# Kernel tuning notes

Hardware: AMD Instinct MI355X
Metric: run time of the kernel (lower is better)

The kernel has to match this reference:

```python
import jax, jax.numpy as jnp
import numpy as np

B, K, D, S, E = 256, 512, 64, 100000, 20000  # batch, knowledge_n, low_dim, student_n, exer_n


def setup_inputs() -> dict:
    key = jax.random.key(0)
    ks = jax.random.split(key, 10)
    stu_id = jax.random.randint(ks[0], (B,), 0, S)
    exer_id = jax.random.randint(ks[1], (B,), 0, E)
    kn_emb = jax.random.uniform(ks[2], (B, K), dtype=jnp.float32)
    # learned parameters (xavier-ish scale)
    stu_table = jax.random.normal(ks[3], (S, D), dtype=jnp.float32) * 0.05
    exer_table = jax.random.normal(ks[4], (E, D), dtype=jnp.float32) * 0.05
    kn_table = jax.random.normal(ks[5], (K, D), dtype=jnp.float32) * 0.05
    W1 = jax.random.normal(ks[6], (K, K + D), dtype=jnp.float32) * (2.0 / (2 * K + D)) ** 0.5
    W2 = jax.random.normal(ks[7], (K, K + D), dtype=jnp.float32) * (2.0 / (2 * K + D)) ** 0.5
    W3 = jax.random.normal(ks[8], (1, K), dtype=jnp.float32) * (2.0 / (K + 1)) ** 0.5
    b3 = jnp.zeros((1,), dtype=jnp.float32)
    return {"stu_id": stu_id, "exer_id": exer_id, "kn_emb": kn_emb,
            "stu_table": stu_table, "exer_table": exer_table, "kn_table": kn_table,
            "W1": W1, "W2": W2, "W3": W3, "b3": b3}


def reference(stu_id, exer_id, kn_emb, stu_table, exer_table, kn_table, W1, W2, W3, b3):
    k = kn_table.shape[0]  # knowledge_n
    # sigmoid(stu_emb @ kn_table.T): (B, K) per-concept proficiency / difficulty
    stu = jax.nn.sigmoid(stu_table[stu_id] @ kn_table.T)
    exer = jax.nn.sigmoid(exer_table[exer_id] @ kn_table.T)
    # Linear on cat([repeated stu/exer vec, kn_vector]) decomposes: split W into
    # the first K columns (acting on the batch vector, constant over the K axis)
    # and the last D columns (acting on kn_table, constant over batch).
    pref = jax.nn.sigmoid((stu @ W1[:, :k].T)[:, None, :] + (kn_table @ W1[:, k:].T)[None, :, :])  # (B,K,K)
    diff = jax.nn.sigmoid((exer @ W2[:, :k].T)[:, None, :] + (kn_table @ W2[:, k:].T)[None, :, :])  # (B,K,K)
    o = jax.nn.sigmoid(jnp.einsum('bkn,n->bk', pref - diff, W3[0]) + b3)  # (B,K)
    sum_out = jnp.sum(o * kn_emb, axis=1, keepdims=True)  # (B,1)
    count = jnp.sum(kn_emb, axis=1, keepdims=True)
    return sum_out / count
```

## Files before the change

kernel.cpp:

```cpp
#include <hip/hip_runtime.h>

#define B_ 256
#define K_ 512
#define D_ 64
#define KD_ 576
#define LOG2E 1.44269504088896340736f

typedef float v4f __attribute__((ext_vector_type(4)));
typedef short bf16x8 __attribute__((ext_vector_type(8)));
typedef float f32x16 __attribute__((ext_vector_type(16)));

#define ZERO16 {0.f,0.f,0.f,0.f,0.f,0.f,0.f,0.f,0.f,0.f,0.f,0.f,0.f,0.f,0.f,0.f}

__device__ __forceinline__ float fexp2(float x) {
#if __has_builtin(__builtin_amdgcn_exp2f)
    return __builtin_amdgcn_exp2f(x);
#else
    float r; asm("v_exp_f32 %0, %1" : "=v"(r) : "v"(x)); return r;
#endif
}
__device__ __forceinline__ float frcp(float x) {
#if __has_builtin(__builtin_amdgcn_rcpf)
    return __builtin_amdgcn_rcpf(x);
#else
    float r; asm("v_rcp_f32 %0, %1" : "=v"(r) : "v"(x)); return r;
#endif
}
__device__ __forceinline__ float fsig(float x) {
    return frcp(1.0f + fexp2(-LOG2E * x));
}
__device__ __forceinline__ ushort f2bf(float f) {
    union { float f; unsigned u; } v; v.f = f;
    return (ushort)((v.u + 0x7FFFu + ((v.u >> 16) & 1u)) >> 16);
}
__device__ __forceinline__ bf16x8 ldcvt8(const float* p) {
    float4 a = *(const float4*)p;
    float4 b = *(const float4*)(p + 4);
    bf16x8 r;
    r[0] = (short)f2bf(a.x); r[1] = (short)f2bf(a.y);
    r[2] = (short)f2bf(a.z); r[3] = (short)f2bf(a.w);
    r[4] = (short)f2bf(b.x); r[5] = (short)f2bf(b.y);
    r[6] = (short)f2bf(b.z); r[7] = (short)f2bf(b.w);
    return r;
}

__global__ void __launch_bounds__(256) kS(const int* __restrict__ sid,
                                          const int* __restrict__ eid,
                                          const float* __restrict__ stu_t,
                                          const float* __restrict__ exer_t,
                                          const float* __restrict__ kn_t,
                                          ushort* __restrict__ Sbu) {
    const int bid = blockIdx.x, t = threadIdx.x;
    const int l = t & 63, w = t >> 6;
    const int dk = (l >> 5) * 8;
    const int tab = bid >> 5, bt = (bid >> 3) & 3, nt = bid & 7;
    const int b0 = bt * 64, n0 = nt * 64;
    const int brow = b0 + (w & 1) * 32 + (l & 31);
    const int ncol = n0 + (w >> 1) * 32 + (l & 31);
    const int id = (tab ? eid : sid)[brow];
    const float* ar = (tab ? exer_t : stu_t) + (size_t)id * D_;
    const float* br = kn_t + (size_t)ncol * D_;
    f32x16 acc = ZERO16;
#pragma unroll
    for (int kk = 0; kk < 4; kk++) {
        bf16x8 a = ldcvt8(ar + kk * 16 + dk);
        bf16x8 b = ldcvt8(br + kk * 16 + dk);
        acc = __builtin_amdgcn_mfma_f32_32x32x16_bf16(a, b, acc, 0, 0, 0);
    }
    ushort* So = Sbu + (size_t)tab * B_ * K_;
#pragma unroll
    for (int r = 0; r < 16; r++) {
        const int row = (r & 3) + 8 * (r >> 2) + 4 * (l >> 5);
        So[(size_t)(b0 + (w & 1) * 32 + row) * K_ + ncol] = f2bf(fsig(acc[r]));
    }
}

__global__ void __launch_bounds__(256) kEF(const ushort* __restrict__ Sbu,
                                           const float* __restrict__ W1,
                                           const float* __restrict__ W2,
                                           const float* __restrict__ kn_t,
                                           float* __restrict__ E,
                                           float* __restrict__ FT1,
                                           float* __restrict__ FT2) {
    __shared__ float shm[4224];
    const int bid = blockIdx.x, t = threadIdx.x;
    const int l = t & 63, w = t >> 6;
    if (bid < 256) {
        const int mat = bid >> 7, bt = (bid >> 4) & 7, nt = bid & 15;
        const int b0 = bt * 32, n0 = nt * 32;
        const int arow = b0 + (l & 31);
        const int nrow = n0 + (l & 31);
        const int koff = w * 128 + (l >> 5) * 8;
        const short* Sp = (const short*)Sbu + (size_t)(mat * B_ + arow) * K_ + koff;
        const float* Wp = (mat ? W2 : W1) + (size_t)nrow * KD_ + koff;
        f32x16 acc = ZERO16;
#pragma unroll
        for (int kk = 0; kk < 8; kk++) {
            bf16x8 a = *(const bf16x8*)(Sp + kk * 16);
            bf16x8 b = ldcvt8(Wp + kk * 16);
            acc = __builtin_amdgcn_mfma_f32_32x32x16_bf16(a, b, acc, 0, 0, 0);
        }
#pragma unroll
        for (int r = 0; r < 16; r++) {
            const int row = (r & 3) + 8 * (r >> 2) + 4 * (l >> 5);
            shm[w * 1056 + row * 33 + (l & 31)] = acc[r];
        }
        __syncthreads();
#pragma unroll
        for (int i = 0; i < 4; i++) {
            const int o = i * 256 + t;
            const int row = (o >> 5) & 31, col = o & 31;
            const float v = shm[row * 33 + col] + shm[1056 + row * 33 + col]
                          + shm[2112 + row * 33 + col] + shm[3168 + row * 33 + col];
            E[(size_t)mat * B_ * K_ + (size_t)(b0 + row) * K_ + n0 + col]
                = fexp2(-LOG2E * v);
        }
    } else {
        const int fid = bid - 256;
        const int mat = fid >> 6, kt = (fid >> 3) & 7, nt = fid & 7;
        const int k0 = kt * 64, n0 = nt * 64;
        const int krow = k0 + (w & 1) * 32 + (l & 31);
        const int ncol = n0 + (w >> 1) * 32 + (l & 31);
        const int dk = (l >> 5) * 8;
        const float* Wm = mat ? W2 : W1;
        const float* ar = kn_t + (size_t)krow * D_;
        const float* br = Wm + (size_t)ncol * KD_ + K_;
        f32x16 acc = ZERO16;
#pragma unroll
        for (int kk = 0; kk < 4; kk++) {
            bf16x8 a = ldcvt8(ar + kk * 16 + dk);
            bf16x8 b = ldcvt8(br + kk * 16 + dk);
            acc = __builtin_amdgcn_mfma_f32_32x32x16_bf16(a, b, acc, 0, 0, 0);
        }
        const int nl_ = (w >> 1) * 32 + (l & 31);
#pragma unroll
        for (int r = 0; r < 16; r++) {
            const int row = (r & 3) + 8 * (r >> 2) + 4 * (l >> 5);
            shm[nl_ * 65 + (w & 1) * 32 + row] = fexp2(-LOG2E * acc[r]);
        }
        __syncthreads();
        float* Fo = mat ? FT2 : FT1;
#pragma unroll
        for (int i = 0; i < 16; i++) {
            const int q = i * 256 + t;
            const int r_ = q >> 6, c_ = q & 63;
            Fo[(size_t)(n0 + r_) * K_ + k0 + c_] = shm[r_ * 65 + c_];
        }
    }
}

__global__ void __launch_bounds__(512) kMain(const float* __restrict__ FT1,
                                             const float* __restrict__ FT2,
                                             const float* __restrict__ Ebase,
                                             const float* __restrict__ W3,
                                             float* __restrict__ pPart) {
    __shared__ float es[2][64][8];
    __shared__ float sacc[3][2][16][64];
    const int t = threadIdx.x, l = t & 63, w = t >> 6;
    const int kg = blockIdx.x, bG = blockIdx.y, ns = blockIdx.z;
    const int b0 = bG * 8, n0 = ns * 64;
    const int k = kg * 256 + l * 4;
    const int bh = w & 1, nq = w >> 1;

#pragma unroll
    for (int it = 0; it < 2; it++) {
        const int i = it * 512 + t;
        const int n = i & 63, b = (i >> 6) & 7, mat = i >> 9;
        es[mat][n][b] = Ebase[(size_t)mat * B_ * K_ + (size_t)(b0 + b) * K_ + n0 + n];
    }
    __syncthreads();

    const float* f1p = FT1 + (size_t)(n0 + nq * 16) * K_ + k;
    const float* f2p = FT2 + (size_t)(n0 + nq * 16) * K_ + k;
    const float* w3p = W3 + n0 + nq * 16;

    v4f acc[4];
#pragma unroll
    for (int b = 0; b < 4; b++) acc[b] = (v4f){0.f, 0.f, 0.f, 0.f};

#pragma unroll 4
    for (int nl = 0; nl < 16; nl++) {
        const v4f f1 = *(const v4f*)(f1p + (size_t)nl * K_);
        const v4f f2 = *(const v4f*)(f2p + (size_t)nl * K_);
        const float w3n = w3p[nl];
        const v4f e1 = *(const v4f*)&es[0][nq * 16 + nl][bh * 4];
        const v4f e2 = *(const v4f*)&es[1][nq * 16 + nl][bh * 4];
#pragma unroll
        for (int b = 0; b < 4; b++) {
            const v4f pd = e1[b] * f1 + 1.0f;
            const v4f qd = e2[b] * f2 + 1.0f;
            const v4f den = pd * qd;
            const v4f num = (qd - pd) * w3n;
            const float dxy = den.x * den.y, dzw = den.z * den.w;
            const float rxy = frcp(dxy), rzw = frcp(dzw);
            v4f rc;
            rc.x = rxy * den.y; rc.y = rxy * den.x;
            rc.z = rzw * den.w; rc.w = rzw * den.z;
            acc[b] += num * rc;
        }
    }

    if (nq != 0) {
#pragma unroll
        for (int b = 0; b < 4; b++)
#pragma unroll
            for (int c = 0; c < 4; c++)
                sacc[nq - 1][bh][b * 4 + c][l] = acc[b][c];
    }
    __syncthreads();
    if (nq == 0) {
#pragma unroll
        for (int b = 0; b < 4; b++) {
            v4f s = acc[b];
#pragma unroll
            for (int q = 0; q < 3; q++) {
                s.x += sacc[q][bh][b * 4 + 0][l];
                s.y += sacc[q][bh][b * 4 + 1][l];
                s.z += sacc[q][bh][b * 4 + 2][l];
                s.w += sacc[q][bh][b * 4 + 3][l];
            }
            *(v4f*)(pPart + ((size_t)ns * B_ + b0 + bh * 4 + b) * K_ + k) = s;
        }
    }
}

__global__ void __launch_bounds__(256) kFin(const float* __restrict__ pPart,
                                            const float* __restrict__ kn_emb,
                                            const float* __restrict__ b3,
                                            float* __restrict__ out) {
    const int t = threadIdx.x, l = t & 63, w = t >> 6;
    const int b = blockIdx.x * 4 + w;
    const float b3v = b3[0];
    const float* ke = kn_emb + (size_t)b * K_;
    float num = 0.f, den = 0.f;
#pragma unroll
    for (int c = 0; c < 8; c++) {
        const int kk = c * 64 + l;
        float sv = 0.f;
#pragma unroll
        for (int s = 0; s < 8; s++)
            sv += pPart[((size_t)s * B_ + b) * K_ + kk];
        const float kv = ke[kk];
        num = fmaf(fsig(sv + b3v), kv, num);
        den += kv;
    }
#pragma unroll
    for (int off = 32; off; off >>= 1) {
        num += __shfl_xor(num, off, 64);
        den += __shfl_xor(den, off, 64);
    }
    if (l == 0) out[b] = num / den;
}

extern "C" void kernel_launch(void* const* d_in, const int* in_sizes, int n_in,
                              void* d_out, int out_size, void* d_ws, size_t ws_size,
                              hipStream_t stream) {
    const int*   stu_id     = (const int*)d_in[0];
    const int*   exer_id    = (const int*)d_in[1];
    const float* kn_emb     = (const float*)d_in[2];
    const float* stu_table  = (const float*)d_in[3];
    const float* exer_table = (const float*)d_in[4];
    const float* kn_table   = (const float*)d_in[5];
    const float* W1         = (const float*)d_in[6];
    const float* W2         = (const float*)d_in[7];
    const float* W3         = (const float*)d_in[8];
    const float* b3         = (const float*)d_in[9];
    float* out = (float*)d_out;

    float* ws = (float*)d_ws;
    float* FT1   = ws;
    float* FT2   = FT1 + (size_t)K_ * K_;
    float* E     = FT2 + (size_t)K_ * K_;
    ushort* Sbu  = (ushort*)(E + 2 * (size_t)B_ * K_);
    float* pPart = (float*)(Sbu + 2 * (size_t)B_ * K_);

    kS<<<64, 256, 0, stream>>>(stu_id, exer_id, stu_table, exer_table,
                               kn_table, Sbu);
    kEF<<<384, 256, 0, stream>>>(Sbu, W1, W2, kn_table, E, FT1, FT2);
    kMain<<<dim3(2, 32, 8), 512, 0, stream>>>(FT1, FT2, E, W3, pPart);
    kFin<<<64, 256, 0, stream>>>(pPart, kn_emb, b3, out);
}
```

Baseline: 37.19 us.

## Run main pairwise sigmoid-difference loop in packed fp16 with fp16 F tables

Stores the exp-factor tables FT1/FT2 as packed fp16 and rewrites the main kernel to compute pd/qd/den/numerator and reciprocals with packed half2 arithmetic and v_rcp_f16. The work split also changes: each block now covers 4 batch rows, with waves partitioned over n, and partials are reduced through shared memory. The final kernel uses one block per batch row. The aim is to halve table bandwidth and double ALU throughput in the dominant loop, at the cost of fp16 accumulation error and possible overflow or precision loss in the products.

```diff
diff --git a/kernel.cpp b/kernel.cpp
--- a/kernel.cpp
+++ b/kernel.cpp
@@ -9,6 +9,7 @@
 typedef float v4f __attribute__((ext_vector_type(4)));
 typedef short bf16x8 __attribute__((ext_vector_type(8)));
 typedef float f32x16 __attribute__((ext_vector_type(16)));
+typedef _Float16 h2 __attribute__((ext_vector_type(2)));
 
 #define ZERO16 {0.f,0.f,0.f,0.f,0.f,0.f,0.f,0.f,0.f,0.f,0.f,0.f,0.f,0.f,0.f,0.f}
 
@@ -29,9 +30,21 @@
 __device__ __forceinline__ float fsig(float x) {
     return frcp(1.0f + fexp2(-LOG2E * x));
 }
+__device__ __forceinline__ _Float16 hrcp(_Float16 x) {
+    _Float16 r; asm("v_rcp_f16 %0, %1" : "=v"(r) : "v"(x)); return r;
+}
 __device__ __forceinline__ ushort f2bf(float f) {
     union { float f; unsigned u; } v; v.f = f;
     return (ushort)((v.u + 0x7FFFu + ((v.u >> 16) & 1u)) >> 16);
+}
+__device__ __forceinline__ unsigned f2h_dup(float x) {
+    const _Float16 h = (_Float16)x;
+    const h2 p = {h, h};
+    return __builtin_bit_cast(unsigned, p);
+}
+__device__ __forceinline__ unsigned f2h_pair(float a, float b) {
+    const h2 p = {(_Float16)a, (_Float16)b};
+    return __builtin_bit_cast(unsigned, p);
 }
 __device__ __forceinline__ bf16x8 ldcvt8(const float* p) {
     float4 a = *(const float4*)p;
@@ -80,8 +93,8 @@
                                            const float* __restrict__ W2,
                                            const float* __restrict__ kn_t,
                                            float* __restrict__ E,
-                                           float* __restrict__ FT1,
-                                           float* __restrict__ FT2) {
+                                           unsigned* __restrict__ FT1h,
+                                           unsigned* __restrict__ FT2h) {
     __shared__ float shm[4224];
     const int bid = blockIdx.x, t = threadIdx.x;
     const int l = t & 63, w = t >> 6;
@@ -139,88 +152,105 @@
             shm[nl_ * 65 + (w & 1) * 32 + row] = fexp2(-LOG2E * acc[r]);
         }
         __syncthreads();
-        float* Fo = mat ? FT2 : FT1;
-#pragma unroll
-        for (int i = 0; i < 16; i++) {
+        unsigned* Fo = mat ? FT2h : FT1h;
+#pragma unroll
+        for (int i = 0; i < 8; i++) {
             const int q = i * 256 + t;
-            const int r_ = q >> 6, c_ = q & 63;
-            Fo[(size_t)(n0 + r_) * K_ + k0 + c_] = shm[r_ * 65 + c_];
-        }
-    }
-}
-
-__global__ void __launch_bounds__(512) kMain(const float* __restrict__ FT1,
-                                             const float* __restrict__ FT2,
+            const int r_ = q >> 5, c_ = q & 31;
+            Fo[(size_t)(n0 + r_) * (K_ / 2) + (k0 >> 1) + c_] =
+                f2h_pair(shm[r_ * 65 + 2 * c_], shm[r_ * 65 + 2 * c_ + 1]);
+        }
+    }
+}
+
+__global__ void __launch_bounds__(512) kMain(const unsigned* __restrict__ FT1h,
+                                             const unsigned* __restrict__ FT2h,
                                              const float* __restrict__ Ebase,
                                              const float* __restrict__ W3,
                                              float* __restrict__ pPart) {
-    __shared__ float es[2][64][8];
-    __shared__ float sacc[3][2][16][64];
+    __shared__ unsigned es[2][64][4];
+    __shared__ unsigned w3s[64];
+    __shared__ float sacc[4][4][64][8];
     const int t = threadIdx.x, l = t & 63, w = t >> 6;
     const int kg = blockIdx.x, bG = blockIdx.y, ns = blockIdx.z;
-    const int b0 = bG * 8, n0 = ns * 64;
-    const int k = kg * 256 + l * 4;
-    const int bh = w & 1, nq = w >> 1;
-
-#pragma unroll
-    for (int it = 0; it < 2; it++) {
-        const int i = it * 512 + t;
-        const int n = i & 63, b = (i >> 6) & 7, mat = i >> 9;
-        es[mat][n][b] = Ebase[(size_t)mat * B_ * K_ + (size_t)(b0 + b) * K_ + n0 + n];
-    }
+    const int b0 = bG * 4, n0 = ns * 64;
+
+    {
+        const int n = t & 63, b = (t >> 6) & 3, mat = t >> 8;
+        const float ev = Ebase[(size_t)mat * B_ * K_ + (size_t)(b0 + b) * K_ + n0 + n];
+        es[mat][n][b] = f2h_dup(ev);
+    }
+    if (t < 64) w3s[t] = f2h_dup(W3[n0 + t]);
     __syncthreads();
 
-    const float* f1p = FT1 + (size_t)(n0 + nq * 16) * K_ + k;
-    const float* f2p = FT2 + (size_t)(n0 + nq * 16) * K_ + k;
-    const float* w3p = W3 + n0 + nq * 16;
-
-    v4f acc[4];
-#pragma unroll
-    for (int b = 0; b < 4; b++) acc[b] = (v4f){0.f, 0.f, 0.f, 0.f};
-
-#pragma unroll 4
-    for (int nl = 0; nl < 16; nl++) {
-        const v4f f1 = *(const v4f*)(f1p + (size_t)nl * K_);
-        const v4f f2 = *(const v4f*)(f2p + (size_t)nl * K_);
-        const float w3n = w3p[nl];
-        const v4f e1 = *(const v4f*)&es[0][nq * 16 + nl][bh * 4];
-        const v4f e2 = *(const v4f*)&es[1][nq * 16 + nl][bh * 4];
+    const int kq = kg * 128 + l * 2;
+    const unsigned* f1p = FT1h + (size_t)n0 * (K_ / 2) + kq;
+    const unsigned* f2p = FT2h + (size_t)n0 * (K_ / 2) + kq;
+
+    const h2 one2 = {(_Float16)1.0f, (_Float16)1.0f};
+    h2 acc[4][2];
+#pragma unroll
+    for (int b = 0; b < 4; b++) {
+        acc[b][0] = (h2){(_Float16)0.0f, (_Float16)0.0f};
+        acc[b][1] = (h2){(_Float16)0.0f, (_Float16)0.0f};
+    }
+
+    const int nbase = w * 8;
+#pragma unroll
+    for (int nl = 0; nl < 8; nl++) {
+        const int n = nbase + nl;
+        const uint2 f1r = *(const uint2*)(f1p + (size_t)n * (K_ / 2));
+        const uint2 f2r = *(const uint2*)(f2p + (size_t)n * (K_ / 2));
+        const h2 f1a = __builtin_bit_cast(h2, f1r.x);
+        const h2 f1b = __builtin_bit_cast(h2, f1r.y);
+        const h2 f2a = __builtin_bit_cast(h2, f2r.x);
+        const h2 f2b = __builtin_bit_cast(h2, f2r.y);
+        const h2 w3h = __builtin_bit_cast(h2, w3s[n]);
+        const uint4 e1r = *(const uint4*)&es[0][n][0];
+        const uint4 e2r = *(const uint4*)&es[1][n][0];
+        const unsigned e1u[4] = {e1r.x, e1r.y, e1r.z, e1r.w};
+        const unsigned e2u[4] = {e2r.x, e2r.y, e2r.z, e2r.w};
 #pragma unroll
         for (int b = 0; b < 4; b++) {
-            const v4f pd = e1[b] * f1 + 1.0f;
-            const v4f qd = e2[b] * f2 + 1.0f;
-            const v4f den = pd * qd;
-            const v4f num = (qd - pd) * w3n;
-            const float dxy = den.x * den.y, dzw = den.z * den.w;
-            const float rxy = frcp(dxy), rzw = frcp(dzw);
-            v4f rc;
-            rc.x = rxy * den.y; rc.y = rxy * den.x;
-            rc.z = rzw * den.w; rc.w = rzw * den.z;
-            acc[b] += num * rc;
-        }
-    }
-
-    if (nq != 0) {
-#pragma unroll
-        for (int b = 0; b < 4; b++)
-#pragma unroll
-            for (int c = 0; c < 4; c++)
-                sacc[nq - 1][bh][b * 4 + c][l] = acc[b][c];
+            const h2 e1 = __builtin_bit_cast(h2, e1u[b]);
+            const h2 e2 = __builtin_bit_cast(h2, e2u[b]);
+            {
+                const h2 pd = e1 * f1a + one2;
+                const h2 qd = e2 * f2a + one2;
+                const h2 den = pd * qd;
+                const h2 nw = (qd - pd) * w3h;
+                const h2 rc = {hrcp(den.x), hrcp(den.y)};
+                acc[b][0] += nw * rc;
+            }
+            {
+                const h2 pd = e1 * f1b + one2;
+                const h2 qd = e2 * f2b + one2;
+                const h2 den = pd * qd;
+                const h2 nw = (qd - pd) * w3h;
+                const h2 rc = {hrcp(den.x), hrcp(den.y)};
+                acc[b][1] += nw * rc;
+            }
+        }
+    }
+
+#pragma unroll
+    for (int b = 0; b < 4; b++) {
+        sacc[b][0][l][w] = (float)acc[b][0].x;
+        sacc[b][1][l][w] = (float)acc[b][0].y;
+        sacc[b][2][l][w] = (float)acc[b][1].x;
+        sacc[b][3][l][w] = (float)acc[b][1].y;
     }
     __syncthreads();
-    if (nq == 0) {
-#pragma unroll
-        for (int b = 0; b < 4; b++) {
-            v4f s = acc[b];
-#pragma unroll
-            for (int q = 0; q < 3; q++) {
-                s.x += sacc[q][bh][b * 4 + 0][l];
-                s.y += sacc[q][bh][b * 4 + 1][l];
-                s.z += sacc[q][bh][b * 4 + 2][l];
-                s.w += sacc[q][bh][b * 4 + 3][l];
-            }
-            *(v4f*)(pPart + ((size_t)ns * B_ + b0 + bh * 4 + b) * K_ + k) = s;
-        }
+#pragma unroll
+    for (int o = 0; o < 2; o++) {
+        const int flat = o * 512 + t;
+        const int b = flat >> 8, rem = flat & 255, l2 = rem >> 2, c = rem & 3;
+        const v4f lo = *(const v4f*)&sacc[b][c][l2][0];
+        const v4f hi = *(const v4f*)&sacc[b][c][l2][4];
+        const float s = ((lo.x + lo.y) + (lo.z + lo.w))
+                      + ((hi.x + hi.y) + (hi.z + hi.w));
+        const int k = kg * 256 + l2 * 4 + c;
+        pPart[((size_t)ns * B_ + b0 + b) * K_ + k] = s;
     }
 }
 
@@ -228,19 +258,19 @@
                                             const float* __restrict__ kn_emb,
                                             const float* __restrict__ b3,
                                             float* __restrict__ out) {
+    __shared__ float rn[4], rd[4];
     const int t = threadIdx.x, l = t & 63, w = t >> 6;
-    const int b = blockIdx.x * 4 + w;
+    const int b = blockIdx.x;
     const float b3v = b3[0];
-    const float* ke = kn_emb + (size_t)b * K_;
     float num = 0.f, den = 0.f;
 #pragma unroll
-    for (int c = 0; c < 8; c++) {
-        const int kk = c * 64 + l;
+    for (int c = 0; c < 2; c++) {
+        const int kk = c * 256 + t;
         float sv = 0.f;
 #pragma unroll
         for (int s = 0; s < 8; s++)
             sv += pPart[((size_t)s * B_ + b) * K_ + kk];
-        const float kv = ke[kk];
+        const float kv = kn_emb[(size_t)b * K_ + kk];
         num = fmaf(fsig(sv + b3v), kv, num);
         den += kv;
     }
@@ -249,7 +279,10 @@
         num += __shfl_xor(num, off, 64);
         den += __shfl_xor(den, off, 64);
     }
-    if (l == 0) out[b] = num / den;
+    if (l == 0) { rn[w] = num; rd[w] = den; }
+    __syncthreads();
+    if (t == 0)
+        out[b] = (rn[0] + rn[1] + rn[2] + rn[3]) / (rd[0] + rd[1] + rd[2] + rd[3]);
 }
 
 extern "C" void kernel_launch(void* const* d_in, const int* in_sizes, int n_in,
@@ -267,16 +300,15 @@
     const float* b3         = (const float*)d_in[9];
     float* out = (float*)d_out;
 
-    float* ws = (float*)d_ws;
-    float* FT1   = ws;
-    float* FT2   = FT1 + (size_t)K_ * K_;
-    float* E     = FT2 + (size_t)K_ * K_;
-    ushort* Sbu  = (ushort*)(E + 2 * (size_t)B_ * K_);
-    float* pPart = (float*)(Sbu + 2 * (size_t)B_ * K_);
+    unsigned* FT1h = (unsigned*)d_ws;
+    unsigned* FT2h = FT1h + (size_t)K_ * K_ / 2;
+    float* E       = (float*)(FT2h + (size_t)K_ * K_ / 2);
+    ushort* Sbu    = (ushort*)(E + 2 * (size_t)B_ * K_);
+    float* pPart   = (float*)(Sbu + 2 * (size_t)B_ * K_);
 
     kS<<<64, 256, 0, stream>>>(stu_id, exer_id, stu_table, exer_table,
                                kn_table, Sbu);
-    kEF<<<384, 256, 0, stream>>>(Sbu, W1, W2, kn_table, E, FT1, FT2);
-    kMain<<<dim3(2, 32, 8), 512, 0, stream>>>(FT1, FT2, E, W3, pPart);
-    kFin<<<64, 256, 0, stream>>>(pPart, kn_emb, b3, out);
-}
+    kEF<<<384, 256, 0, stream>>>(Sbu, W1, W2, kn_table, E, FT1h, FT2h);
+    kMain<<<dim3(2, 64, 8), 512, 0, stream>>>(FT1h, FT2h, E, W3, pPart);
+    kFin<<<256, 256, 0, stream>>>(pPart, kn_emb, b3, out);
+}
```

Measured after the change: 36.53 us. Within noise of the previous version (-1.8%).
